# Optimization experiments

Measured on AMD Instinct MI355X. Metric: run time of the kernel, lower is better.

## Reference

```python
import jax, jax.numpy as jnp
import numpy as np

EPS = 1e-5

def setup_inputs() -> dict:
    key = jax.random.key(0)
    ks = jax.random.split(key, 8)
    B, C, H, W = 8, 128, 128, 128
    return {
        "x1": jax.random.normal(ks[0], (B, C, H, W), jnp.float32),
        "x2": jax.random.normal(ks[1], (B, C, H, W), jnp.float32),
        "se_w1": jax.random.normal(ks[2], (C // 4, 2 * C), jnp.float32) * 0.05,
        "se_w2": jax.random.normal(ks[3], (2 * C, C // 4), jnp.float32) * 0.05,
        "conv_w": jax.random.normal(ks[4], (C, 2 * C, 3, 3), jnp.float32) * 0.05,
        "bn_gamma": jnp.ones((C,), jnp.float32),
        "bn_beta": jnp.zeros((C,), jnp.float32),
        "bn_mean": jax.random.normal(ks[5], (C,), jnp.float32) * 0.1,
        "bn_var": jax.random.uniform(ks[6], (C,), jnp.float32, 0.5, 1.5),
        "gamma": jax.random.uniform(ks[7], (1,), jnp.float32),
    }

def reference(x1, x2, se_w1, se_w2, conv_w, bn_gamma, bn_beta, bn_mean, bn_var, gamma):
    B, C, H, W = x1.shape
    x = jnp.concatenate([x1, x2], axis=1)                      # [B,2C,H,W]
    # SE gate: global avg pool -> Linear/ReLU/Linear/Sigmoid
    avg = jnp.mean(x, axis=(2, 3))                             # [B,2C]
    h = jax.nn.relu(avg @ se_w1.T)                             # [B,C//4]
    se = jax.nn.sigmoid(h @ se_w2.T)                           # [B,2C]
    x = x * se[:, :, None, None]
    # ConvBNReLU (3x3, pad 1, eval-mode BN)
    x = jax.lax.conv_general_dilated(
        x, conv_w, window_strides=(1, 1), padding="SAME",
        dimension_numbers=("NCHW", "OIHW", "NCHW"))           # [B,C,H,W]
    inv = bn_gamma / jnp.sqrt(bn_var + EPS)
    x = jax.nn.relu(x * inv[None, :, None, None]
                    + (bn_beta - bn_mean * inv)[None, :, None, None])
    # Channel self-attention with max-subtraction trick
    q = x.reshape(B, C, H * W)                                 # query = key = value
    sim = jnp.einsum("bcn,bdn->bcd", q, q)                     # [B,C,C]
    sim = jnp.max(sim, axis=-1, keepdims=True) - sim
    sim = jax.nn.softmax(sim, axis=-1)
    feat = jnp.einsum("bcd,bdn->bcn", sim, q).reshape(B, C, H, W)
    return gamma * feat + x
```

## Files before the change

kernel.cpp:

```cpp
#include <hip/hip_runtime.h>
#include <math.h>

#define B_   8
#define C_   128
#define C2_  256
#define H_   128
#define W_   128
#define HW_  16384
#define CR_  32
#define EPS_ 1e-5f
#define NS_  32

typedef _Float16 f16;
typedef f16 f16x8 __attribute__((ext_vector_type(8)));
typedef f16 f16x4 __attribute__((ext_vector_type(4)));
typedef float f32x4 __attribute__((ext_vector_type(4)));

__global__ __launch_bounds__(256) void prep_kernel(
    const float* __restrict__ x1, const float* __restrict__ x2,
    const float* __restrict__ conv_w,
    float* __restrict__ avgp, f16* __restrict__ xs, f16* __restrict__ wt,
    float* __restrict__ zp)
{
    __shared__ f16 T[W_ * 136];
    __shared__ float part[C2_];
    int h = blockIdx.x, b = blockIdx.y;
    int tid = threadIdx.x;
    if (h == 0 && b == 0 && tid < 128) zp[tid] = 0.f;
    f16* out = xs + ((size_t)b * H_ + h) * W_ * C2_;
    for (int p = 0; p < 2; ++p) {
        const float* src = p ? x2 : x1;
        __syncthreads();
        for (int idx = tid; idx < C_ * 32; idx += 256) {
            int c = idx >> 5, w4 = (idx & 31) << 2;
            const float4 v = *(const float4*)&src[(((size_t)b * C_ + c) * H_ + h) * W_ + w4];
            float s = v.x + v.y + v.z + v.w;
            s += __shfl_xor(s, 1, 64);  s += __shfl_xor(s, 2, 64);
            s += __shfl_xor(s, 4, 64);  s += __shfl_xor(s, 8, 64);
            s += __shfl_xor(s, 16, 64);
            if ((tid & 31) == 0) part[p * C_ + c] = s;
            int cs = c ^ (8 * ((idx & 31) & 15));
            T[(w4 + 0) * 136 + cs] = (f16)v.x;
            T[(w4 + 1) * 136 + cs] = (f16)v.y;
            T[(w4 + 2) * 136 + cs] = (f16)v.z;
            T[(w4 + 3) * 136 + cs] = (f16)v.w;
        }
        __syncthreads();
        for (int u = tid; u < W_ * 16; u += 256) {
            int w = u >> 4, o = u & 15;
            f16x8 v = *(const f16x8*)&T[w * 136 + ((o * 8) ^ (8 * ((w >> 2) & 15)))];
            *(f16x8*)&out[w * C2_ + p * C_ + o * 8] = v;
        }
    }
    __syncthreads();
    avgp[((size_t)h * B_ + b) * C2_ + tid] = part[tid];
    {
        int base = (b * H_ + h) * 288;
        for (int i = tid; i < 288; i += 256) {
            int idx = base + i;
            int ci = idx & 31;
            int co = (idx >> 5) & 127;
            int tt = idx >> 12;
            int cc = tt / 9, t = tt - cc * 9;
            wt[idx] = (f16)conv_w[((size_t)co * C2_ + cc * 32 + ci) * 9 + t];
        }
    }
}

__global__ __launch_bounds__(256) void se_mlp_kernel(
    const float* __restrict__ avgp, const float* __restrict__ w1,
    const float* __restrict__ w2, float* __restrict__ se)
{
    int b = blockIdx.x;
    __shared__ float s_avg[C2_];
    __shared__ float s_h[CR_];
    float s = 0.f;
    for (int h = 0; h < H_; ++h)
        s += avgp[((size_t)h * B_ + b) * C2_ + threadIdx.x];
    s_avg[threadIdx.x] = s * (1.f / (float)HW_);
    __syncthreads();
    {
        int j = threadIdx.x >> 3, sub = threadIdx.x & 7;
        float a = 0.f;
        #pragma unroll 8
        for (int k = sub * 32; k < sub * 32 + 32; ++k) a += s_avg[k] * w1[j * C2_ + k];
        a += __shfl_xor(a, 1, 64); a += __shfl_xor(a, 2, 64); a += __shfl_xor(a, 4, 64);
        if (sub == 0) s_h[j] = fmaxf(a, 0.f);
    }
    __syncthreads();
    float o = 0.f;
    #pragma unroll
    for (int j = 0; j < CR_; ++j) o += s_h[j] * w2[threadIdx.x * CR_ + j];
    se[b * C2_ + threadIdx.x] = 1.f / (1.f + expf(-o));
}

#define WH_F16  9216
#define XH_F16  8320
#define SMEM_BYTES 35584

__device__ __forceinline__ void gload16(const f16* g, f16* l) {
    __builtin_amdgcn_global_load_lds(
        (const __attribute__((address_space(1))) void*)(g),
        (__attribute__((address_space(3))) void*)(l), 16, 0, 0);
}

__global__ __launch_bounds__(256, 4) void conv_mfma_big(
    const f16* __restrict__ xs, const f16* __restrict__ wt,
    const float* __restrict__ se, const f16* __restrict__ zp,
    const float* __restrict__ bn_gamma, const float* __restrict__ bn_beta,
    const float* __restrict__ bn_mean, const float* __restrict__ bn_var,
    f16* __restrict__ yh, f16* __restrict__ yt)
{
    extern __shared__ __align__(16) f16 smem[];
    f16* Ws  = smem;
    f16* Xs  = smem + WH_F16;
    f16* seh = smem + WH_F16 + XH_F16;

    int h0 = blockIdx.x * 2, cy = blockIdx.y, b = blockIdx.z;
    int tid = threadIdx.x;
    int wave = tid >> 6, lane = tid & 63;
    int orow = wave >> 1, nh = wave & 1;
    int lr = lane & 15, kg = lane >> 4;
    const f16* xsb = xs + (size_t)b * ((size_t)H_ * W_ * C2_);

    seh[tid] = (f16)se[b * C2_ + tid];

    f32x4 acc[4][4];
    #pragma unroll
    for (int i = 0; i < 4; ++i)
        #pragma unroll
        for (int j = 0; j < 4; ++j)
            #pragma unroll
            for (int r = 0; r < 4; ++r) acc[i][j][r] = 0.f;

    for (int ph = 0; ph < 16; ++ph) {
        if (ph) __syncthreads();
        int cc = ph >> 1, cio = (ph & 1) * 16;
        #pragma unroll
        for (int k = 0; k < 5; ++k) {
            int u = k * 256 + tid;
            if (u < 1152) {
                int cell = u >> 1, p = u & 1;
                int t = cell >> 6, co_l = cell & 63;
                int hsrc = p ^ ((co_l ^ (co_l >> 2)) & 1);
                gload16(wt + (((size_t)(cc * 9 + t) * 128 + cy * 64 + co_l) << 5)
                           + cio + (hsrc << 3),
                        Ws + u * 8);
            }
        }
        #pragma unroll
        for (int k = 0; k < 5; ++k) {
            int u = k * 256 + tid;
            if (u < 1040) {
                int cell = u >> 1, p = u & 1;
                int r = cell / 130, col = cell - r * 130;
                int hsrc = p ^ ((col ^ (col >> 2)) & 1);
                int gh = h0 - 1 + r, gw = col - 1;
                const f16* src = ((unsigned)gh < (unsigned)H_ && (unsigned)gw < (unsigned)W_)
                    ? xsb + (((size_t)gh << 7) + (size_t)gw) * C2_ + ph * 16 + (hsrc << 3)
                    : zp;
                gload16(src, Xs + u * 8);
            }
        }
        __syncthreads();
        f16x4 sv = *(const f16x4*)&seh[ph * 16 + kg * 4];
        #pragma unroll
        for (int t = 0; t < 9; ++t) {
            const int dh = t / 3, dw = t % 3;
            const int rr = orow + dh;
            f16x4 bf[4];
            #pragma unroll
            for (int j = 0; j < 4; ++j) {
                int col = nh * 64 + j * 16 + lr + dw;
                int pos = kg ^ (((col ^ (col >> 2)) & 1) << 1);
                bf[j] = *(const f16x4*)&Xs[(rr * 130 + col) * 16 + pos * 4];
            }
            #pragma unroll
            for (int i2 = 0; i2 < 4; ++i2) {
                int co_l = i2 * 16 + lr;
                int pos = kg ^ (((co_l ^ (co_l >> 2)) & 1) << 1);
                f16x4 af = *(const f16x4*)&Ws[(t * 64 + co_l) * 16 + pos * 4];
                af = af * sv;
                #pragma unroll
                for (int j = 0; j < 4; ++j)
                    acc[i2][j] = __builtin_amdgcn_mfma_f32_16x16x16f16(
                        af, bf[j], acc[i2][j], 0, 0, 0);
            }
        }
    }
    int h = h0 + orow;
    f16x4 tvv[4][4];
    #pragma unroll
    for (int i2 = 0; i2 < 4; ++i2) {
        int cb = cy * 64 + i2 * 16 + kg * 4;
        float inv[4], add[4];
        #pragma unroll
        for (int r = 0; r < 4; ++r) {
            int c = cb + r;
            inv[r] = bn_gamma[c] * rsqrtf(bn_var[c] + EPS_);
            add[r] = bn_beta[c] - bn_mean[c] * inv[r];
        }
        #pragma unroll
        for (int j = 0; j < 4; ++j) {
            int n = nh * 64 + j * 16 + lr;
            f16x4 tv;
            #pragma unroll
            for (int r = 0; r < 4; ++r) {
                float v = fmaxf(acc[i2][j][r] * inv[r] + add[r], 0.f);
                tv[r] = (f16)v;
                yh[((size_t)b * C_ + cb + r) * HW_ + h * W_ + n] = (f16)v;
            }
            tvv[i2][j] = tv;
        }
    }
    f16* T = smem;
    for (int ro = 0; ro < 2; ++ro) {
        __syncthreads();
        if (orow == ro) {
            #pragma unroll
            for (int i2 = 0; i2 < 4; ++i2)
                #pragma unroll
                for (int j = 0; j < 4; ++j)
                    *(f16x4*)&T[(nh * 64 + j * 16 + lr) * 72 + i2 * 16 + kg * 4] = tvv[i2][j];
        }
        __syncthreads();
        for (int u = tid; u < 1024; u += 256) {
            int n = u >> 3, o8 = u & 7;
            *(f16x8*)&yt[((size_t)b * HW_ + (h0 + ro) * W_ + n) * C_ + cy * 64 + o8 * 8] =
                *(const f16x8*)&T[n * 72 + o8 * 8];
        }
    }
}

__global__ __launch_bounds__(512) void sim_mfma_kernel(
    const f16* __restrict__ yh, float* __restrict__ simp)
{
    int ns = blockIdx.x, b = blockIdx.y;
    int tid = threadIdx.x, wave = tid >> 6, lane = tid & 63;
    int wm = wave >> 2, wn = wave & 3;
    int lr = lane & 15, kg = lane >> 4;
    const f16* Y = yh + (size_t)b * C_ * HW_;
    int n0 = ns * (HW_ / NS_);

    f32x4 acc[4][2];
    #pragma unroll
    for (int i = 0; i < 4; ++i)
        #pragma unroll
        for (int j = 0; j < 2; ++j)
            #pragma unroll
            for (int r = 0; r < 4; ++r) acc[i][j][r] = 0.f;

    for (int kk = 0; kk < 16; ++kk) {
        int k = n0 + kk * 32 + kg * 8;
        f16x8 af[4], bf[2];
        #pragma unroll
        for (int i = 0; i < 4; ++i)
            af[i] = *(const f16x8*)&Y[(size_t)(wm * 64 + i * 16 + lr) * HW_ + k];
        #pragma unroll
        for (int j = 0; j < 2; ++j)
            bf[j] = *(const f16x8*)&Y[(size_t)(wn * 32 + j * 16 + lr) * HW_ + k];
        #pragma unroll
        for (int i = 0; i < 4; ++i)
            #pragma unroll
            for (int j = 0; j < 2; ++j)
                acc[i][j] = __builtin_amdgcn_mfma_f32_16x16x32_f16(af[i], bf[j], acc[i][j], 0, 0, 0);
    }
    float* dst = simp + (size_t)(ns * B_ + b) * C_ * C_;
    #pragma unroll
    for (int i = 0; i < 4; ++i)
        #pragma unroll
        for (int j = 0; j < 2; ++j)
            #pragma unroll
            for (int r = 0; r < 4; ++r)
                dst[(wm * 64 + i * 16 + kg * 4 + r) * C_ + wn * 32 + j * 16 + lr] = acc[i][j][r];
}

__global__ __launch_bounds__(128) void softmax_kernel(
    const float* __restrict__ simp, f16* __restrict__ Ph)
{
    int bc = blockIdx.x;
    int b = bc / C_;
    int d = threadIdx.x;
    float s = 0.f;
    for (int ns = 0; ns < NS_; ++ns)
        s += simp[((size_t)(ns * B_ + b) * C_ + (bc % C_)) * C_ + d];
    float v = -s;
    float m = v;
    #pragma unroll
    for (int off = 32; off > 0; off >>= 1) m = fmaxf(m, __shfl_xor(m, off, 64));
    __shared__ float sm[2], ss[2];
    int wid = threadIdx.x >> 6;
    if ((threadIdx.x & 63) == 0) sm[wid] = m;
    __syncthreads();
    m = fmaxf(sm[0], sm[1]);
    float p = expf(v - m);
    float sum = p;
    #pragma unroll
    for (int off = 32; off > 0; off >>= 1) sum += __shfl_xor(sum, off, 64);
    if ((threadIdx.x & 63) == 0) ss[wid] = sum;
    __syncthreads();
    sum = ss[0] + ss[1];
    Ph[(size_t)bc * C_ + d] = (f16)(p / sum);
}

__global__ __launch_bounds__(256) void feat_mfma_kernel(
    const f16* __restrict__ Ph, const f16* __restrict__ yt,
    const f16* __restrict__ yh,
    const float* __restrict__ gamma, float* __restrict__ out)
{
    int nt = blockIdx.x, b = blockIdx.y;
    int tid = threadIdx.x, wave = tid >> 6, lane = tid & 63;
    int wm = wave >> 1, wn = wave & 1;
    int lr = lane & 15, kg = lane >> 4;
    int n0 = nt * 128;
    const f16* Pb = Ph + (size_t)b * C_ * C_;
    const f16* Yt = yt + (size_t)b * HW_ * C_;

    f32x4 acc[4][4];
    #pragma unroll
    for (int i = 0; i < 4; ++i)
        #pragma unroll
        for (int j = 0; j < 4; ++j)
            #pragma unroll
            for (int r = 0; r < 4; ++r) acc[i][j][r] = 0.f;

    #pragma unroll
    for (int kk = 0; kk < 4; ++kk) {
        int k = kk * 32 + kg * 8;
        f16x8 af[4], bf[4];
        #pragma unroll
        for (int i = 0; i < 4; ++i)
            af[i] = *(const f16x8*)&Pb[(wm * 64 + i * 16 + lr) * C_ + k];
        #pragma unroll
        for (int j = 0; j < 4; ++j)
            bf[j] = *(const f16x8*)&Yt[(size_t)(n0 + wn * 64 + j * 16 + lr) * C_ + k];
        #pragma unroll
        for (int i = 0; i < 4; ++i)
            #pragma unroll
            for (int j = 0; j < 4; ++j)
                acc[i][j] = __builtin_amdgcn_mfma_f32_16x16x32_f16(af[i], bf[j], acc[i][j], 0, 0, 0);
    }
    float g = gamma[0];
    #pragma unroll
    for (int i = 0; i < 4; ++i) {
        int cb = wm * 64 + i * 16 + kg * 4;
        #pragma unroll
        for (int j = 0; j < 4; ++j) {
            int n = n0 + wn * 64 + j * 16 + lr;
            #pragma unroll
            for (int r = 0; r < 4; ++r) {
                float res = (float)yh[((size_t)b * C_ + cb + r) * HW_ + n];
                out[((size_t)b * C_ + cb + r) * HW_ + n] = g * acc[i][j][r] + res;
            }
        }
    }
}

extern "C" void kernel_launch(void* const* d_in, const int* in_sizes, int n_in,
                              void* d_out, int out_size, void* d_ws, size_t ws_size,
                              hipStream_t stream)
{
    const float* x1       = (const float*)d_in[0];
    const float* x2       = (const float*)d_in[1];
    const float* se_w1    = (const float*)d_in[2];
    const float* se_w2    = (const float*)d_in[3];
    const float* conv_w   = (const float*)d_in[4];
    const float* bn_gamma = (const float*)d_in[5];
    const float* bn_beta  = (const float*)d_in[6];
    const float* bn_mean  = (const float*)d_in[7];
    const float* bn_var   = (const float*)d_in[8];
    const float* gamma    = (const float*)d_in[9];
    float* out = (float*)d_out;

    char* ws = (char*)d_ws;
    float* zp   = (float*)(ws);
    float* se   = (float*)(ws + 8192);
    f16*   Ph   = (f16*)  (ws + 16384);
    f16*   wt   = (f16*)  (ws + 278528);
    f16*   xs   = (f16*)  (ws + 1048576);
    float* simp = (float*)(ws + 1048576);
    f16*   yh   = (f16*)  (ws + 68157440);
    float* avgp = (float*)(ws + 68157440);
    f16*   yt   = (f16*)  (ws + 101711872);

    prep_kernel<<<dim3(H_, B_), 256, 0, stream>>>(x1, x2, conv_w, avgp, xs, wt, zp);
    se_mlp_kernel<<<dim3(B_), 256, 0, stream>>>(avgp, se_w1, se_w2, se);

    hipFuncSetAttribute((const void*)conv_mfma_big,
        hipFuncAttributeMaxDynamicSharedMemorySize, SMEM_BYTES);
    conv_mfma_big<<<dim3(H_ / 2, 2, B_), 256, SMEM_BYTES, stream>>>(
        xs, wt, se, (const f16*)zp, bn_gamma, bn_beta, bn_mean, bn_var, yh, yt);

    sim_mfma_kernel<<<dim3(NS_, B_), 512, 0, stream>>>(yh, simp);
    softmax_kernel<<<dim3(B_ * C_), 128, 0, stream>>>(simp, Ph);
    feat_mfma_kernel<<<dim3(HW_ / 128, B_), 256, 0, stream>>>(Ph, yt, yh, gamma, out);
}
```

Before: 427.1 us.

## Use 16x16x32 MFMA with channel-blocked input layout and larger K chunks

```diff
diff --git a/kernel.cpp b/kernel.cpp
--- a/kernel.cpp
+++ b/kernel.cpp
@@ -27,7 +27,7 @@
     int h = blockIdx.x, b = blockIdx.y;
     int tid = threadIdx.x;
     if (h == 0 && b == 0 && tid < 128) zp[tid] = 0.f;
-    f16* out = xs + ((size_t)b * H_ + h) * W_ * C2_;
+    f16* xb = xs + (size_t)b * ((size_t)8 * HW_ * 32);
     for (int p = 0; p < 2; ++p) {
         const float* src = p ? x2 : x1;
         __syncthreads();
@@ -49,7 +49,8 @@
         for (int u = tid; u < W_ * 16; u += 256) {
             int w = u >> 4, o = u & 15;
             f16x8 v = *(const f16x8*)&T[w * 136 + ((o * 8) ^ (8 * ((w >> 2) & 15)))];
-            *(f16x8*)&out[w * C2_ + p * C_ + o * 8] = v;
+            int ci = p * C_ + o * 8;
+            *(f16x8*)&xb[(((size_t)(ci >> 5) * H_ + h) * W_ + w) * 32 + (ci & 31)] = v;
         }
     }
     __syncthreads();
@@ -94,9 +95,9 @@
     se[b * C2_ + threadIdx.x] = 1.f / (1.f + expf(-o));
 }
 
-#define WH_F16  9216
-#define XH_F16  8320
-#define SMEM_BYTES 35584
+#define WC_F16  18432
+#define XC_F16  16640
+#define SMEM_BYTES 70656
 
 __device__ __forceinline__ void gload16(const f16* g, f16* l) {
     __builtin_amdgcn_global_load_lds(
@@ -104,7 +105,7 @@
         (__attribute__((address_space(3))) void*)(l), 16, 0, 0);
 }
 
-__global__ __launch_bounds__(256, 4) void conv_mfma_big(
+__global__ __launch_bounds__(256, 2) void conv_mfma_big(
     const f16* __restrict__ xs, const f16* __restrict__ wt,
     const float* __restrict__ se, const f16* __restrict__ zp,
     const float* __restrict__ bn_gamma, const float* __restrict__ bn_beta,
@@ -113,15 +114,14 @@
 {
     extern __shared__ __align__(16) f16 smem[];
     f16* Ws  = smem;
-    f16* Xs  = smem + WH_F16;
-    f16* seh = smem + WH_F16 + XH_F16;
-
-    int h0 = blockIdx.x * 2, cy = blockIdx.y, b = blockIdx.z;
+    f16* Xs  = smem + WC_F16;
+    f16* seh = smem + WC_F16 + XC_F16;
+
+    int cy = blockIdx.x, h0 = blockIdx.y * 2, b = blockIdx.z;
     int tid = threadIdx.x;
     int wave = tid >> 6, lane = tid & 63;
     int orow = wave >> 1, nh = wave & 1;
     int lr = lane & 15, kg = lane >> 4;
-    const f16* xsb = xs + (size_t)b * ((size_t)H_ * W_ * C2_);
 
     seh[tid] = (f16)se[b * C2_ + tid];
 
@@ -133,57 +133,48 @@
             #pragma unroll
             for (int r = 0; r < 4; ++r) acc[i][j][r] = 0.f;
 
-    for (int ph = 0; ph < 16; ++ph) {
-        if (ph) __syncthreads();
-        int cc = ph >> 1, cio = (ph & 1) * 16;
-        #pragma unroll
-        for (int k = 0; k < 5; ++k) {
+    for (int cc = 0; cc < 8; ++cc) {
+        if (cc) __syncthreads();
+        const f16* wsrc = wt + ((size_t)(cc * 9) * 128 + cy * 64) * 32;
+        #pragma unroll
+        for (int k = 0; k < 9; ++k) {
             int u = k * 256 + tid;
-            if (u < 1152) {
-                int cell = u >> 1, p = u & 1;
-                int t = cell >> 6, co_l = cell & 63;
-                int hsrc = p ^ ((co_l ^ (co_l >> 2)) & 1);
-                gload16(wt + (((size_t)(cc * 9 + t) * 128 + cy * 64 + co_l) << 5)
-                           + cio + (hsrc << 3),
-                        Ws + u * 8);
-            }
-        }
-        #pragma unroll
-        for (int k = 0; k < 5; ++k) {
+            int row = u >> 2, g = u & 3;
+            int t = row >> 6, col = row & 63;
+            gload16(wsrc + (((size_t)t * 128 + col) << 5) + (g << 3),
+                    Ws + u * 8);
+        }
+        const f16* xsc = xs + ((size_t)b * 8 + cc) * ((size_t)HW_ * 32);
+        #pragma unroll
+        for (int k = 0; k < 9; ++k) {
             int u = k * 256 + tid;
-            if (u < 1040) {
-                int cell = u >> 1, p = u & 1;
+            if (u < 2080) {
+                int cell = u >> 2, g = u & 3;
                 int r = cell / 130, col = cell - r * 130;
-                int hsrc = p ^ ((col ^ (col >> 2)) & 1);
                 int gh = h0 - 1 + r, gw = col - 1;
                 const f16* src = ((unsigned)gh < (unsigned)H_ && (unsigned)gw < (unsigned)W_)
-                    ? xsb + (((size_t)gh << 7) + (size_t)gw) * C2_ + ph * 16 + (hsrc << 3)
+                    ? xsc + (((size_t)gh * W_ + gw) << 5) + (g << 3)
                     : zp;
                 gload16(src, Xs + u * 8);
             }
         }
         __syncthreads();
-        f16x4 sv = *(const f16x4*)&seh[ph * 16 + kg * 4];
+        f16x8 sv = *(const f16x8*)&seh[cc * 32 + kg * 8];
         #pragma unroll
         for (int t = 0; t < 9; ++t) {
             const int dh = t / 3, dw = t % 3;
             const int rr = orow + dh;
-            f16x4 bf[4];
-            #pragma unroll
-            for (int j = 0; j < 4; ++j) {
-                int col = nh * 64 + j * 16 + lr + dw;
-                int pos = kg ^ (((col ^ (col >> 2)) & 1) << 1);
-                bf[j] = *(const f16x4*)&Xs[(rr * 130 + col) * 16 + pos * 4];
-            }
+            f16x8 bf[4];
+            #pragma unroll
+            for (int j = 0; j < 4; ++j)
+                bf[j] = *(const f16x8*)&Xs[((rr * 130 + nh * 64 + j * 16 + lr + dw) << 5) + kg * 8];
             #pragma unroll
             for (int i2 = 0; i2 < 4; ++i2) {
-                int co_l = i2 * 16 + lr;
-                int pos = kg ^ (((co_l ^ (co_l >> 2)) & 1) << 1);
-                f16x4 af = *(const f16x4*)&Ws[(t * 64 + co_l) * 16 + pos * 4];
+                f16x8 af = *(const f16x8*)&Ws[((t * 64 + i2 * 16 + lr) << 5) + kg * 8];
                 af = af * sv;
                 #pragma unroll
                 for (int j = 0; j < 4; ++j)
-                    acc[i2][j] = __builtin_amdgcn_mfma_f32_16x16x16f16(
+                    acc[i2][j] = __builtin_amdgcn_mfma_f32_16x16x32_f16(
                         af, bf[j], acc[i2][j], 0, 0, 0);
             }
         }
@@ -388,7 +379,7 @@
 
     hipFuncSetAttribute((const void*)conv_mfma_big,
         hipFuncAttributeMaxDynamicSharedMemorySize, SMEM_BYTES);
-    conv_mfma_big<<<dim3(H_ / 2, 2, B_), 256, SMEM_BYTES, stream>>>(
+    conv_mfma_big<<<dim3(2, H_ / 2, B_), 256, SMEM_BYTES, stream>>>(
         xs, wt, se, (const f16*)zp, bn_gamma, bn_beta, bn_mean, bn_var, yh, yt);
 
     sim_mfma_kernel<<<dim3(NS_, B_), 512, 0, stream>>>(yh, simp);
```

Result: faster. 352.9 us (-17.4%).
